# Performance work log

Hardware: AMD Instinct MI355X
Metric: run time of the kernel (lower is better)

Reference implementation:

```python
import jax, jax.numpy as jnp
import numpy as np

DIM = 768
HEADS = 12
HEAD_DIM = DIM // HEADS
HIDDEN = 4 * DIM
EPS = 1e-5


def _ln(x, w, b):
    mu = jnp.mean(x, axis=-1, keepdims=True)
    var = jnp.var(x, axis=-1, keepdims=True)
    return (x - mu) * jax.lax.rsqrt(var + EPS) * w + b


def setup_inputs() -> dict:
    key = jax.random.key(0)
    ks = jax.random.split(key, 8)
    B, N, C = 8, 1024, DIM
    s = 0.02
    return {
        "before": jax.random.normal(ks[0], (B, N, C), jnp.float32),
        "after": jax.random.normal(ks[1], (B, N, C), jnp.float32),
        "norm1_w": jnp.ones((C,), jnp.float32),
        "norm1_b": jnp.zeros((C,), jnp.float32),
        "qkv_w": jax.random.normal(ks[2], (3 * C, C), jnp.float32) * s,
        "hln_w": jnp.ones((HEAD_DIM,), jnp.float32),
        "hln_b": jnp.zeros((HEAD_DIM,), jnp.float32),
        "proj_w": jax.random.normal(ks[3], (C, C), jnp.float32) * s,
        "proj_b": jnp.zeros((C,), jnp.float32),
        "norm2_w": jnp.ones((C,), jnp.float32),
        "norm2_b": jnp.zeros((C,), jnp.float32),
        "fc1_w": jax.random.normal(ks[4], (HIDDEN, C), jnp.float32) * s,
        "fc1_b": jnp.zeros((HIDDEN,), jnp.float32),
        "fc2_w": jax.random.normal(ks[5], (C, HIDDEN), jnp.float32) * s,
        "fc2_b": jnp.zeros((C,), jnp.float32),
    }


def _qkv_normed(x, qkv_w, hln_w, hln_b):
    B, N, C = x.shape
    qkv = x @ qkv_w.T  # (B,N,3C)
    qkv = qkv.reshape(B, N, 3, HEADS, HEAD_DIM).transpose(2, 0, 3, 1, 4)  # (3,B,H,N,hd)
    qkv = _ln(qkv, hln_w, hln_b)  # per-head LayerNorm over head_dim
    return qkv[0], qkv[1], qkv[2]


def _cross_attn(q, k, v, proj_w, proj_b):
    B, H, N, D = q.shape
    scale = D ** (-0.5)
    attn = jax.nn.softmax(jnp.einsum("bhnd,bhmd->bhnm", q, k) * scale, axis=-1)
    ctx = jnp.einsum("bhnm,bhmd->bhnd", attn, v)
    ctx = ctx.transpose(0, 2, 1, 3).reshape(B, N, H * D)
    ctx = ctx @ proj_w.T + proj_b
    # NOTE: original adds q.reshape(B,N,C) WITHOUT transposing heads (faithful)
    return ctx + q.reshape(B, N, H * D)


def _mlp(x, fc1_w, fc1_b, fc2_w, fc2_b):
    h = jax.nn.gelu(x @ fc1_w.T + fc1_b, approximate=False)
    return h @ fc2_w.T + fc2_b


def reference(before, after, norm1_w, norm1_b, qkv_w, hln_w, hln_b, proj_w, proj_b,
              norm2_w, norm2_b, fc1_w, fc1_b, fc2_w, fc2_b):
    before_n = _ln(before, norm1_w, norm1_b)
    after_n = _ln(after, norm1_w, norm1_b)
    q_b, k_b, v_b = _qkv_normed(before_n, qkv_w, hln_w, hln_b)
    q_a, k_a, v_a = _qkv_normed(after_n, qkv_w, hln_w, hln_b)
    context_a = _cross_attn(q_b, k_a, v_a, proj_w, proj_b)  # before attends to after
    context_b = _cross_attn(q_a, k_b, v_b, proj_w, proj_b)  # after attends to before
    before_o = before_n + context_b
    after_o = after_n + context_a
    before_o = before_o + _mlp(_ln(before_o, norm2_w, norm2_b), fc1_w, fc1_b, fc2_w, fc2_b)
    after_o = after_o + _mlp(_ln(after_o, norm2_w, norm2_b), fc1_w, fc1_b, fc2_w, fc2_b)
    return (before_o, after_o)
```

## Files before the change

kernel.cpp:

```cpp
#include <hip/hip_runtime.h>
#include <hip/hip_bf16.h>

typedef unsigned short u16;
typedef __attribute__((ext_vector_type(8))) short bf16x8;
typedef __attribute__((ext_vector_type(4))) float f32x4;

#define DIRSTRIDE 6291456

__device__ __forceinline__ u16 f2bf(float x){
  __hip_bfloat16 h = __float2bfloat16(x);
  return *reinterpret_cast<u16*>(&h);
}
__device__ __forceinline__ float bf2f(u16 u){
  return __uint_as_float(((unsigned int)u) << 16);
}
__device__ __forceinline__ u16 f2bf_fast(float x){
  return (u16)((__float_as_uint(x) + 0x8000u) >> 16);
}

__device__ __forceinline__ void xcd_remap(int& bx, int& by){
  int gx = (int)gridDim.x;
  int lin = (int)blockIdx.x + gx*(int)blockIdx.y;
  int nwg8 = (gx*(int)gridDim.y) >> 3;
  int rl = (lin & 7)*nwg8 + (lin >> 3);
  bx = rl % gx; by = rl / gx;
}

__global__ __launch_bounds__(256) void zero_kernel(float* __restrict__ p, int n){
  int i = blockIdx.x*256 + threadIdx.x;
  if (i < n) p[i] = 0.f;
}

__global__ __launch_bounds__(256) void cvt_kernel(const float* __restrict__ s,
                                                  u16* __restrict__ d, int n){
  int i = blockIdx.x*256 + threadIdx.x;
  if (i < n) d[i] = f2bf(s[i]);
}

__global__ __launch_bounds__(256) void ln_kernel(const float* __restrict__ s0,
    const float* __restrict__ s1, const float* __restrict__ w,
    const float* __restrict__ b, u16* __restrict__ out,
    float* __restrict__ mu_out, float* __restrict__ rs_out){
  int r = blockIdx.x;
  const float* src = (r < 8192) ? (s0 + (size_t)r*768) : (s1 + (size_t)(r-8192)*768);
  int t = threadIdx.x;
  float v0 = src[t], v1 = src[t+256], v2 = src[t+512];
  __shared__ float red[4];
  float s = v0+v1+v2;
  #pragma unroll
  for (int o=32;o;o>>=1) s += __shfl_xor(s,o);
  if ((t&63)==0) red[t>>6] = s;
  __syncthreads();
  float mean = (red[0]+red[1]+red[2]+red[3]) * (1.0f/768.0f);
  float d0=v0-mean, d1=v1-mean, d2=v2-mean;
  float q = d0*d0+d1*d1+d2*d2;
  __syncthreads();
  #pragma unroll
  for (int o=32;o;o>>=1) q += __shfl_xor(q,o);
  if ((t&63)==0) red[t>>6] = q;
  __syncthreads();
  float var = (red[0]+red[1]+red[2]+red[3]) * (1.0f/768.0f);
  float rstd = rsqrtf(var + 1e-5f);
  if (mu_out && t == 0){ mu_out[r] = mean; rs_out[r] = rstd; }
  size_t base = (size_t)r*768;
  out[base+t]     = f2bf(d0*rstd*w[t]     + b[t]);
  out[base+t+256] = f2bf(d1*rstd*w[t+256] + b[t+256]);
  out[base+t+512] = f2bf(d2*rstd*w[t+512] + b[t+512]);
}

__device__ __forceinline__ void stage_tile64(const u16* g, size_t strideK, u16* lds,
                                             int w, int lane){
  #pragma unroll
  for (int i=0;i<4;i++){
    int row = w*32 + i*8 + (lane>>3);
    int cs  = (lane&7) ^ (row&7);
    const u16* gp = g + (size_t)row*strideK + cs*8;
    __builtin_amdgcn_global_load_lds(
        (const __attribute__((address_space(1))) unsigned int*)gp,
        (__attribute__((address_space(3))) unsigned int*)(lds + (w*4+i)*512),
        16, 0, 0);
  }
}

__device__ __forceinline__ void stage_tile64x64(const u16* g, size_t strideK,
                                                u16* lds, int w, int lane){
  #pragma unroll
  for (int i=0;i<2;i++){
    int row = w*16 + i*8 + (lane>>3);
    int cs  = (lane&7) ^ (row&7);
    const u16* gp = g + (size_t)row*strideK + cs*8;
    __builtin_amdgcn_global_load_lds(
        (const __attribute__((address_space(1))) unsigned int*)gp,
        (__attribute__((address_space(3))) unsigned int*)(lds + (w*2+i)*512),
        16, 0, 0);
  }
}

#define SWZ_FRAG(tile, r, c) (*(const bf16x8*)&(tile)[(r)*64 + (((c) ^ ((r)&7)))*8])

template<int EPI>
__global__ __launch_bounds__(256, 4) void gemm_kernel(
    const u16* __restrict__ A, const u16* __restrict__ W, void* Cout,
    const float* __restrict__ bias, const float* resF,
    int M, int N, int K)
{
  __shared__ __attribute__((aligned(16))) u16 sA[128*64];
  __shared__ __attribute__((aligned(16))) u16 sB[128*64];
  int t = threadIdx.x;
  int w = t>>6, lane = t&63, ln = lane&15, quad = lane>>4;
  int bx, by; xcd_remap(bx, by);
  int m0 = by*128, n0 = bx*128;
  int wr = (w>>1)*64, wc = (w&1)*64;
  f32x4 acc[4][4];
  #pragma unroll
  for (int mi=0;mi<4;mi++)
    #pragma unroll
    for (int ni=0;ni<4;ni++) acc[mi][ni] = (f32x4){0.f,0.f,0.f,0.f};
  int KB = K >> 6;
  for (int kb=0;kb<KB;kb++){
    __syncthreads();
    stage_tile64(A + (size_t)m0*K + kb*64, K, sA, w, lane);
    stage_tile64(W + (size_t)n0*K + kb*64, K, sB, w, lane);
    __syncthreads();
    #pragma unroll
    for (int ks=0;ks<2;ks++){
      bf16x8 aF[4], bF[4];
      #pragma unroll
      for (int mi=0;mi<4;mi++) aF[mi] = SWZ_FRAG(sA, wr+mi*16+ln, ks*4+quad);
      #pragma unroll
      for (int ni=0;ni<4;ni++) bF[ni] = SWZ_FRAG(sB, wc+ni*16+ln, ks*4+quad);
      #pragma unroll
      for (int mi=0;mi<4;mi++)
        #pragma unroll
        for (int ni=0;ni<4;ni++)
          acc[mi][ni] = __builtin_amdgcn_mfma_f32_16x16x32_bf16(aF[mi], bF[ni], acc[mi][ni], 0,0,0);
    }
  }
  #pragma unroll
  for (int mi=0;mi<4;mi++){
    #pragma unroll
    for (int ni=0;ni<4;ni++){
      #pragma unroll
      for (int r=0;r<4;r++){
        int row = m0 + wr + mi*16 + quad*4 + r;
        int col = n0 + wc + ni*16 + ln;
        size_t ridx = (size_t)row*N + col;
        float v = acc[mi][ni][r];
        if (EPI == 2){
          v += bias[col];
          v = 0.5f*v*(1.0f + erff(v*0.70710678118654752f));
          ((u16*)Cout)[ridx] = f2bf(v);
        } else {
          float rf = resF[ridx];
          ((float*)Cout)[ridx] = v + bias[col] + rf;
        }
      }
    }
  }
}

__global__ __launch_bounds__(256, 4) void gemm_fc2_kernel(
    const u16* __restrict__ A, const u16* __restrict__ W, float* __restrict__ Cout,
    const float* __restrict__ bias, const float* resF)
{
  const int N = 768, K = 3072, KB = 48;
  __shared__ __attribute__((aligned(16))) u16 sA[128*64];
  __shared__ __attribute__((aligned(16))) u16 sB[64*64];
  int t = threadIdx.x;
  int w = t>>6, lane = t&63, ln = lane&15, quad = lane>>4;
  int bx, by; xcd_remap(bx, by);
  int m0 = by*128, n0 = bx*64;
  int wr = w*32;
  f32x4 acc[2][4];
  #pragma unroll
  for (int mi=0;mi<2;mi++)
    #pragma unroll
    for (int ni=0;ni<4;ni++) acc[mi][ni] = (f32x4){0.f,0.f,0.f,0.f};
  for (int kb=0;kb<KB;kb++){
    __syncthreads();
    stage_tile64(A + (size_t)m0*K + kb*64, K, sA, w, lane);
    stage_tile64x64(W + (size_t)n0*K + kb*64, K, sB, w, lane);
    __syncthreads();
    #pragma unroll
    for (int ks=0;ks<2;ks++){
      bf16x8 aF[2], bF[4];
      #pragma unroll
      for (int mi=0;mi<2;mi++) aF[mi] = SWZ_FRAG(sA, wr+mi*16+ln, ks*4+quad);
      #pragma unroll
      for (int ni=0;ni<4;ni++) bF[ni] = SWZ_FRAG(sB, ni*16+ln, ks*4+quad);
      #pragma unroll
      for (int mi=0;mi<2;mi++)
        #pragma unroll
        for (int ni=0;ni<4;ni++)
          acc[mi][ni] = __builtin_amdgcn_mfma_f32_16x16x32_bf16(aF[mi], bF[ni], acc[mi][ni], 0,0,0);
    }
  }
  #pragma unroll
  for (int mi=0;mi<2;mi++){
    #pragma unroll
    for (int ni=0;ni<4;ni++){
      #pragma unroll
      for (int r=0;r<4;r++){
        int row = m0 + wr + mi*16 + quad*4 + r;
        int col = n0 + ni*16 + ln;
        size_t ridx = (size_t)row*N + col;
        float rf = resF[ridx];
        Cout[ridx] = acc[mi][ni][r] + bias[col] + rf;
      }
    }
  }
}

__global__ __launch_bounds__(256, 4) void gemm_proj_kernel(
    const u16* __restrict__ A, const u16* __restrict__ W, float* Cout,
    const float* __restrict__ bias, const u16* __restrict__ resQ,
    const float* __restrict__ before, const float* __restrict__ after,
    const float* __restrict__ n1w, const float* __restrict__ n1b,
    const float* __restrict__ mu, const float* __restrict__ rstd)
{
  const int K = 768, N = 768, KB = 12;
  __shared__ __attribute__((aligned(16))) u16 sA[128*64];
  __shared__ __attribute__((aligned(16))) u16 sB[128*64];
  int t = threadIdx.x;
  int w = t>>6, lane = t&63, ln = lane&15, quad = lane>>4;
  int bx, by; xcd_remap(bx, by);
  int m0 = by*128, n0 = bx*128;
  int wr = (w>>1)*64, wc = (w&1)*64;
  f32x4 acc[4][4];
  #pragma unroll
  for (int mi=0;mi<4;mi++)
    #pragma unroll
    for (int ni=0;ni<4;ni++) acc[mi][ni] = (f32x4){0.f,0.f,0.f,0.f};
  for (int kb=0;kb<KB;kb++){
    __syncthreads();
    stage_tile64(A + (size_t)m0*K + kb*64, K, sA, w, lane);
    stage_tile64(W + (size_t)n0*K + kb*64, K, sB, w, lane);
    __syncthreads();
    #pragma unroll
    for (int ks=0;ks<2;ks++){
      bf16x8 aF[4], bF[4];
      #pragma unroll
      for (int mi=0;mi<4;mi++) aF[mi] = SWZ_FRAG(sA, wr+mi*16+ln, ks*4+quad);
      #pragma unroll
      for (int ni=0;ni<4;ni++) bF[ni] = SWZ_FRAG(sB, wc+ni*16+ln, ks*4+quad);
      #pragma unroll
      for (int mi=0;mi<4;mi++)
        #pragma unroll
        for (int ni=0;ni<4;ni++)
          acc[mi][ni] = __builtin_amdgcn_mfma_f32_16x16x32_bf16(aF[mi], bF[ni], acc[mi][ni], 0,0,0);
    }
  }
  #pragma unroll
  for (int mi=0;mi<4;mi++){
    #pragma unroll
    for (int ni=0;ni<4;ni++){
      #pragma unroll
      for (int r=0;r<4;r++){
        int row = m0 + wr + mi*16 + quad*4 + r;
        int col = n0 + wc + ni*16 + ln;
        size_t ridx = (size_t)row*N + col;
        int dirout = row >> 13;
        int rem = row & 8191;
        size_t qidx = (size_t)(1-dirout)*DIRSTRIDE + (size_t)rem*768 + col;
        const float* src = dirout ? after : before;
        float xr = (src[(size_t)rem*768 + col] - mu[row]) * rstd[row] * n1w[col] + n1b[col];
        Cout[ridx] = acc[mi][ni][r] + bias[col] + bf2f(resQ[qidx]) + xr;
      }
    }
  }
}

__global__ __launch_bounds__(256, 4) void gemm_qkv_kernel(
    const u16* __restrict__ A, const u16* __restrict__ W,
    const float* __restrict__ hw, const float* __restrict__ hb,
    u16* __restrict__ q, u16* __restrict__ k, u16* __restrict__ vt)
{
  const int K = 768, KB = 12;
  __shared__ __attribute__((aligned(16))) u16 sA[128*64];
  __shared__ __attribute__((aligned(16))) u16 sB[128*64];
  int t = threadIdx.x;
  int w = t>>6, lane = t&63, ln = lane&15, quad = lane>>4;
  int bx, by; xcd_remap(bx, by);
  int m0 = by*128, n0 = bx*128;
  int wr = (w>>1)*64, wc = (w&1)*64;
  f32x4 acc[4][4];
  #pragma unroll
  for (int mi=0;mi<4;mi++)
    #pragma unroll
    for (int ni=0;ni<4;ni++) acc[mi][ni] = (f32x4){0.f,0.f,0.f,0.f};
  for (int kb=0;kb<KB;kb++){
    __syncthreads();
    stage_tile64(A + (size_t)m0*K + kb*64, K, sA, w, lane);
    stage_tile64(W + (size_t)n0*K + kb*64, K, sB, w, lane);
    __syncthreads();
    #pragma unroll
    for (int ks=0;ks<2;ks++){
      bf16x8 aF[4], bF[4];
      #pragma unroll
      for (int mi=0;mi<4;mi++) aF[mi] = SWZ_FRAG(sA, wr+mi*16+ln, ks*4+quad);
      #pragma unroll
      for (int ni=0;ni<4;ni++) bF[ni] = SWZ_FRAG(sB, wc+ni*16+ln, ks*4+quad);
      #pragma unroll
      for (int mi=0;mi<4;mi++)
        #pragma unroll
        for (int ni=0;ni<4;ni++)
          acc[mi][ni] = __builtin_amdgcn_mfma_f32_16x16x32_bf16(aF[mi], bF[ni], acc[mi][ni], 0,0,0);
    }
  }
  int sec = (n0 + wc) >> 6;
  int which = sec / 12, h = sec - which*12;
  float hwv[4], hbv[4];
  #pragma unroll
  for (int ni=0;ni<4;ni++){ hwv[ni] = hw[ni*16+ln]; hbv[ni] = hb[ni*16+ln]; }
  #pragma unroll
  for (int mi=0;mi<4;mi++){
    #pragma unroll
    for (int r=0;r<4;r++){
      float s = acc[mi][0][r]+acc[mi][1][r]+acc[mi][2][r]+acc[mi][3][r];
      #pragma unroll
      for (int ofs=1; ofs<16; ofs<<=1) s += __shfl_xor(s, ofs);
      float mu = s * (1.0f/64.0f);
      float vv = 0.f;
      #pragma unroll
      for (int ni=0;ni<4;ni++){ float d = acc[mi][ni][r]-mu; vv += d*d; }
      #pragma unroll
      for (int ofs=1; ofs<16; ofs<<=1) vv += __shfl_xor(vv, ofs);
      float rstd = rsqrtf(vv*(1.0f/64.0f) + 1e-5f);
      int token = m0 + wr + mi*16 + quad*4 + r;
      int dir = token >> 13, bb = (token>>10)&7, n = token & 1023;
      size_t base = (size_t)dir*DIRSTRIDE + (size_t)bb*786432 + (size_t)h*65536;
      #pragma unroll
      for (int ni=0;ni<4;ni++){
        u16 y = f2bf((acc[mi][ni][r]-mu)*rstd*hwv[ni] + hbv[ni]);
        int hd = ni*16 + ln;
        if (which == 0)      q[base + (size_t)n*64 + hd] = y;
        else if (which == 1) k[base + (size_t)n*64 + hd] = y;
        else                 vt[base + (size_t)hd*1024 + n] = y;
      }
    }
  }
}

__global__ __launch_bounds__(256) void flash_kernel(const u16* __restrict__ qg,
    const u16* __restrict__ kg, const u16* __restrict__ vtg, u16* __restrict__ ctx)
{
  __shared__ __attribute__((aligned(16))) u16 sK[2][64*64];
  __shared__ __attribute__((aligned(16))) u16 sV[2][64*64];
  __shared__ __attribute__((aligned(16))) u16 sP[4*16*72];
  int lin = (int)blockIdx.x + 16*((int)blockIdx.y + 96*(int)blockIdx.z);
  int x8 = lin & 7, jj = lin >> 3;
  int qt = jj & 15;
  int g  = x8 + 8*(jj >> 4);
  int dout = g & 1, bh = g >> 1;
  int b = bh/12, h = bh - b*12;
  size_t qbase = (size_t)(1-dout)*DIRSTRIDE + (size_t)b*786432 + (size_t)h*65536;
  size_t kbase = (size_t)dout*DIRSTRIDE + (size_t)b*786432 + (size_t)h*65536;
  int t = threadIdx.x;
  int w = t>>6, lane = t&63, ln = lane&15, quad = lane>>4;
  const u16* qp = qg + qbase + (size_t)(qt*64 + w*16 + ln)*64 + quad*8;
  bf16x8 aQ0 = *(const bf16x8*)qp;
  bf16x8 aQ1 = *(const bf16x8*)(qp + 32);
  bf16x8 vOne;
  #pragma unroll
  for (int j=0;j<8;j++) vOne[j] = (short)0x3F80;
  f32x4 o[4];
  #pragma unroll
  for (int ni=0;ni<4;ni++) o[ni] = (f32x4){0.f,0.f,0.f,0.f};
  f32x4 oL = (f32x4){0.f,0.f,0.f,0.f};
  u16* pw = &sP[w*16*72];
  const float cs = 0.18033688011112042f;
  stage_tile64x64(kg  + kbase, 64, sK[0], w, lane);
  stage_tile64x64(vtg + kbase, 1024, sV[0], w, lane);
  __syncthreads();
  int cur = 0;
  for (int kt=0;kt<16;kt++){
    if (kt < 15){
      stage_tile64x64(kg  + kbase + (size_t)(kt+1)*4096, 64, sK[cur^1], w, lane);
      stage_tile64x64(vtg + kbase + (size_t)(kt+1)*64, 1024, sV[cur^1], w, lane);
    }
    const u16* sKc = sK[cur];
    const u16* sVc = sV[cur];
    bf16x8 bK[4][2], bV[4][2];
    #pragma unroll
    for (int ni=0;ni<4;ni++){
      int rr = ni*16 + ln;
      bK[ni][0] = SWZ_FRAG(sKc, rr, quad);
      bK[ni][1] = SWZ_FRAG(sKc, rr, 4+quad);
      bV[ni][0] = SWZ_FRAG(sVc, rr, quad);
      bV[ni][1] = SWZ_FRAG(sVc, rr, 4+quad);
    }
    f32x4 s[4];
    __builtin_amdgcn_s_setprio(1);
    #pragma unroll
    for (int ni=0;ni<4;ni++){
      s[ni] = (f32x4){0.f,0.f,0.f,0.f};
      s[ni] = __builtin_amdgcn_mfma_f32_16x16x32_bf16(aQ0, bK[ni][0], s[ni], 0,0,0);
      s[ni] = __builtin_amdgcn_mfma_f32_16x16x32_bf16(aQ1, bK[ni][1], s[ni], 0,0,0);
    }
    __builtin_amdgcn_s_setprio(0);
    #pragma unroll
    for (int ni=0;ni<4;ni++){
      #pragma unroll
      for (int r=0;r<4;r++){
        float p = exp2f(s[ni][r]*cs);
        pw[(quad*4+r)*72 + ni*16 + ln] = f2bf_fast(p);
      }
    }
    bf16x8 aP0 = *(const bf16x8*)&pw[ln*72 + quad*8];
    bf16x8 aP1 = *(const bf16x8*)&pw[ln*72 + 32 + quad*8];
    __builtin_amdgcn_s_setprio(1);
    #pragma unroll
    for (int ni=0;ni<4;ni++){
      o[ni] = __builtin_amdgcn_mfma_f32_16x16x32_bf16(aP0, bV[ni][0], o[ni], 0,0,0);
      o[ni] = __builtin_amdgcn_mfma_f32_16x16x32_bf16(aP1, bV[ni][1], o[ni], 0,0,0);
    }
    oL = __builtin_amdgcn_mfma_f32_16x16x32_bf16(aP0, vOne, oL, 0,0,0);
    oL = __builtin_amdgcn_mfma_f32_16x16x32_bf16(aP1, vOne, oL, 0,0,0);
    __builtin_amdgcn_s_setprio(0);
    __syncthreads();
    cur ^= 1;
  }
  #pragma unroll
  for (int ni=0;ni<4;ni++){
    #pragma unroll
    for (int r=0;r<4;r++){
      int row = qt*64 + w*16 + quad*4 + r;
      float val = o[ni][r] / oL[r];
      ctx[((size_t)dout*8192 + (size_t)b*1024 + row)*768 + h*64 + ni*16 + ln] = f2bf(val);
    }
  }
}

extern "C" void kernel_launch(void* const* d_in, const int* in_sizes, int n_in,
                              void* d_out, int out_size, void* d_ws, size_t ws_size,
                              hipStream_t stream)
{
  const float* before = (const float*)d_in[0];
  const float* after  = (const float*)d_in[1];
  const float* n1w  = (const float*)d_in[2];
  const float* n1b  = (const float*)d_in[3];
  const float* qkvw = (const float*)d_in[4];
  const float* hlnw = (const float*)d_in[5];
  const float* hlnb = (const float*)d_in[6];
  const float* projw= (const float*)d_in[7];
  const float* projb= (const float*)d_in[8];
  const float* n2w  = (const float*)d_in[9];
  const float* n2b  = (const float*)d_in[10];
  const float* fc1w = (const float*)d_in[11];
  const float* fc1b = (const float*)d_in[12];
  const float* fc2w = (const float*)d_in[13];
  const float* fc2b = (const float*)d_in[14];

  const size_t REQUIRED = 114950144;
  if (ws_size < REQUIRED){
    zero_kernel<<<(out_size + 255)/256, 256, 0, stream>>>((float*)d_out, out_size);
    return;
  }

  char* ws = (char*)d_ws;
  u16* xn    = (u16*)(ws + 0);
  u16* ctxb  = (u16*)(ws + 0);
  u16* gbuf  = (u16*)(ws + 0);
  u16* qb    = (u16*)(ws + 25165824);
  u16* kb    = (u16*)(ws + 50331648);
  u16* h1n   = (u16*)(ws + 50331648);
  u16* vtb   = (u16*)(ws + 75497472);
  u16* wqkv  = (u16*)(ws + 100663296);
  u16* wproj = (u16*)(ws + 104202240);
  u16* wfc1  = (u16*)(ws + 105381888);
  u16* wfc2  = (u16*)(ws + 110100480);
  float* mu1  = (float*)(ws + 114819072);
  float* rs1  = (float*)(ws + 114884608);
  float* h1   = (float*)d_out;
  float* outp = (float*)d_out;

  cvt_kernel<<<6912, 256, 0, stream>>>(qkvw, wqkv, 1769472);
  cvt_kernel<<<2304, 256, 0, stream>>>(projw, wproj, 589824);
  cvt_kernel<<<9216, 256, 0, stream>>>(fc1w, wfc1, 2359296);
  cvt_kernel<<<9216, 256, 0, stream>>>(fc2w, wfc2, 2359296);

  ln_kernel<<<16384, 256, 0, stream>>>(before, after, n1w, n1b, xn, mu1, rs1);
  gemm_qkv_kernel<<<dim3(18,128), 256, 0, stream>>>(xn, wqkv, hlnw, hlnb, qb, kb, vtb);
  flash_kernel<<<dim3(16,96,2), 256, 0, stream>>>(qb, kb, vtb, ctxb);
  gemm_proj_kernel<<<dim3(6,128), 256, 0, stream>>>(ctxb, wproj, h1,
      projb, qb, before, after, n1w, n1b, mu1, rs1);
  ln_kernel<<<16384, 256, 0, stream>>>(h1, h1 + (size_t)8192*768, n2w, n2b, h1n,
      nullptr, nullptr);
  for (int c = 0; c < 2; c++){
    size_t off = (size_t)c * 8192 * 768;
    gemm_kernel<2><<<dim3(24,64), 256, 0, stream>>>(h1n + off, wfc1, gbuf,
        fc1b, nullptr, 8192, 3072, 768);
    gemm_fc2_kernel<<<dim3(12,64), 256, 0, stream>>>(gbuf, wfc2, outp + off,
        fc2b, h1 + off);
  }
}
```

Before: 648.2 us.

## Double query rows per wave in flash attention to reuse K/V tiles

Each wave now handles 32 query rows (two 16-row MFMA tiles) instead of 16, so each block covers 128 queries and the grid halves. Every K/V tile staged into LDS and every fragment read feeds twice as many MFMAs, halving K/V global and LDS traffic per query. The output normalization now multiplies by a reciprocal instead of dividing per element. In exchange, register use (accumulators, scores) and the sP buffer double, which may lower occupancy, and the halved block count (1536) reduces parallelism.

```diff
diff --git a/kernel.cpp b/kernel.cpp
--- a/kernel.cpp
+++ b/kernel.cpp
@@ -346,28 +346,34 @@
 {
   __shared__ __attribute__((aligned(16))) u16 sK[2][64*64];
   __shared__ __attribute__((aligned(16))) u16 sV[2][64*64];
-  __shared__ __attribute__((aligned(16))) u16 sP[4*16*72];
-  int lin = (int)blockIdx.x + 16*((int)blockIdx.y + 96*(int)blockIdx.z);
+  __shared__ __attribute__((aligned(16))) u16 sP[4*32*72];
+  int lin = (int)blockIdx.x + 8*((int)blockIdx.y + 96*(int)blockIdx.z);
   int x8 = lin & 7, jj = lin >> 3;
-  int qt = jj & 15;
-  int g  = x8 + 8*(jj >> 4);
+  int qt = jj & 7;
+  int g  = x8 + 8*(jj >> 3);
   int dout = g & 1, bh = g >> 1;
   int b = bh/12, h = bh - b*12;
   size_t qbase = (size_t)(1-dout)*DIRSTRIDE + (size_t)b*786432 + (size_t)h*65536;
   size_t kbase = (size_t)dout*DIRSTRIDE + (size_t)b*786432 + (size_t)h*65536;
   int t = threadIdx.x;
   int w = t>>6, lane = t&63, ln = lane&15, quad = lane>>4;
-  const u16* qp = qg + qbase + (size_t)(qt*64 + w*16 + ln)*64 + quad*8;
-  bf16x8 aQ0 = *(const bf16x8*)qp;
-  bf16x8 aQ1 = *(const bf16x8*)(qp + 32);
+  const u16* qp = qg + qbase + (size_t)(qt*128 + w*32 + ln)*64 + quad*8;
+  bf16x8 aQ[2][2];
+  aQ[0][0] = *(const bf16x8*)qp;
+  aQ[0][1] = *(const bf16x8*)(qp + 32);
+  aQ[1][0] = *(const bf16x8*)(qp + 16*64);
+  aQ[1][1] = *(const bf16x8*)(qp + 16*64 + 32);
   bf16x8 vOne;
   #pragma unroll
   for (int j=0;j<8;j++) vOne[j] = (short)0x3F80;
-  f32x4 o[4];
-  #pragma unroll
-  for (int ni=0;ni<4;ni++) o[ni] = (f32x4){0.f,0.f,0.f,0.f};
-  f32x4 oL = (f32x4){0.f,0.f,0.f,0.f};
-  u16* pw = &sP[w*16*72];
+  f32x4 o[2][4], oL[2];
+  #pragma unroll
+  for (int mi=0;mi<2;mi++){
+    #pragma unroll
+    for (int ni=0;ni<4;ni++) o[mi][ni] = (f32x4){0.f,0.f,0.f,0.f};
+    oL[mi] = (f32x4){0.f,0.f,0.f,0.f};
+  }
+  u16* pw = &sP[w*32*72];
   const float cs = 0.18033688011112042f;
   stage_tile64x64(kg  + kbase, 64, sK[0], w, lane);
   stage_tile64x64(vtg + kbase, 1024, sV[0], w, lane);
@@ -380,53 +386,72 @@
     }
     const u16* sKc = sK[cur];
     const u16* sVc = sV[cur];
-    bf16x8 bK[4][2], bV[4][2];
+    bf16x8 bK[4][2];
     #pragma unroll
     for (int ni=0;ni<4;ni++){
       int rr = ni*16 + ln;
       bK[ni][0] = SWZ_FRAG(sKc, rr, quad);
       bK[ni][1] = SWZ_FRAG(sKc, rr, 4+quad);
+    }
+    f32x4 s[2][4];
+    __builtin_amdgcn_s_setprio(1);
+    #pragma unroll
+    for (int mi=0;mi<2;mi++){
+      #pragma unroll
+      for (int ni=0;ni<4;ni++){
+        s[mi][ni] = (f32x4){0.f,0.f,0.f,0.f};
+        s[mi][ni] = __builtin_amdgcn_mfma_f32_16x16x32_bf16(aQ[mi][0], bK[ni][0], s[mi][ni], 0,0,0);
+        s[mi][ni] = __builtin_amdgcn_mfma_f32_16x16x32_bf16(aQ[mi][1], bK[ni][1], s[mi][ni], 0,0,0);
+      }
+    }
+    __builtin_amdgcn_s_setprio(0);
+    bf16x8 bV[4][2];
+    #pragma unroll
+    for (int ni=0;ni<4;ni++){
+      int rr = ni*16 + ln;
       bV[ni][0] = SWZ_FRAG(sVc, rr, quad);
       bV[ni][1] = SWZ_FRAG(sVc, rr, 4+quad);
     }
-    f32x4 s[4];
+    #pragma unroll
+    for (int mi=0;mi<2;mi++)
+      #pragma unroll
+      for (int ni=0;ni<4;ni++)
+        #pragma unroll
+        for (int r=0;r<4;r++){
+          float p = exp2f(s[mi][ni][r]*cs);
+          pw[(mi*16 + quad*4 + r)*72 + ni*16 + ln] = f2bf_fast(p);
+        }
+    bf16x8 aP[2][2];
+    #pragma unroll
+    for (int mi=0;mi<2;mi++){
+      aP[mi][0] = *(const bf16x8*)&pw[(mi*16+ln)*72 + quad*8];
+      aP[mi][1] = *(const bf16x8*)&pw[(mi*16+ln)*72 + 32 + quad*8];
+    }
     __builtin_amdgcn_s_setprio(1);
     #pragma unroll
-    for (int ni=0;ni<4;ni++){
-      s[ni] = (f32x4){0.f,0.f,0.f,0.f};
-      s[ni] = __builtin_amdgcn_mfma_f32_16x16x32_bf16(aQ0, bK[ni][0], s[ni], 0,0,0);
-      s[ni] = __builtin_amdgcn_mfma_f32_16x16x32_bf16(aQ1, bK[ni][1], s[ni], 0,0,0);
+    for (int mi=0;mi<2;mi++){
+      #pragma unroll
+      for (int ni=0;ni<4;ni++){
+        o[mi][ni] = __builtin_amdgcn_mfma_f32_16x16x32_bf16(aP[mi][0], bV[ni][0], o[mi][ni], 0,0,0);
+        o[mi][ni] = __builtin_amdgcn_mfma_f32_16x16x32_bf16(aP[mi][1], bV[ni][1], o[mi][ni], 0,0,0);
+      }
+      oL[mi] = __builtin_amdgcn_mfma_f32_16x16x32_bf16(aP[mi][0], vOne, oL[mi], 0,0,0);
+      oL[mi] = __builtin_amdgcn_mfma_f32_16x16x32_bf16(aP[mi][1], vOne, oL[mi], 0,0,0);
     }
     __builtin_amdgcn_s_setprio(0);
-    #pragma unroll
-    for (int ni=0;ni<4;ni++){
-      #pragma unroll
-      for (int r=0;r<4;r++){
-        float p = exp2f(s[ni][r]*cs);
-        pw[(quad*4+r)*72 + ni*16 + ln] = f2bf_fast(p);
-      }
-    }
-    bf16x8 aP0 = *(const bf16x8*)&pw[ln*72 + quad*8];
-    bf16x8 aP1 = *(const bf16x8*)&pw[ln*72 + 32 + quad*8];
-    __builtin_amdgcn_s_setprio(1);
-    #pragma unroll
-    for (int ni=0;ni<4;ni++){
-      o[ni] = __builtin_amdgcn_mfma_f32_16x16x32_bf16(aP0, bV[ni][0], o[ni], 0,0,0);
-      o[ni] = __builtin_amdgcn_mfma_f32_16x16x32_bf16(aP1, bV[ni][1], o[ni], 0,0,0);
-    }
-    oL = __builtin_amdgcn_mfma_f32_16x16x32_bf16(aP0, vOne, oL, 0,0,0);
-    oL = __builtin_amdgcn_mfma_f32_16x16x32_bf16(aP1, vOne, oL, 0,0,0);
-    __builtin_amdgcn_s_setprio(0);
     __syncthreads();
     cur ^= 1;
   }
   #pragma unroll
-  for (int ni=0;ni<4;ni++){
+  for (int mi=0;mi<2;mi++){
     #pragma unroll
     for (int r=0;r<4;r++){
-      int row = qt*64 + w*16 + quad*4 + r;
-      float val = o[ni][r] / oL[r];
-      ctx[((size_t)dout*8192 + (size_t)b*1024 + row)*768 + h*64 + ni*16 + ln] = f2bf(val);
+      float inv = 1.0f / oL[mi][r];
+      int row = qt*128 + w*32 + mi*16 + quad*4 + r;
+      size_t obase = ((size_t)dout*8192 + (size_t)b*1024 + row)*768 + h*64;
+      #pragma unroll
+      for (int ni=0;ni<4;ni++)
+        ctx[obase + ni*16 + ln] = f2bf(o[mi][ni][r] * inv);
     }
   }
 }
@@ -481,7 +506,7 @@
 
   ln_kernel<<<16384, 256, 0, stream>>>(before, after, n1w, n1b, xn, mu1, rs1);
   gemm_qkv_kernel<<<dim3(18,128), 256, 0, stream>>>(xn, wqkv, hlnw, hlnb, qb, kb, vtb);
-  flash_kernel<<<dim3(16,96,2), 256, 0, stream>>>(qb, kb, vtb, ctxb);
+  flash_kernel<<<dim3(8,96,2), 256, 0, stream>>>(qb, kb, vtb, ctxb);
   gemm_proj_kernel<<<dim3(6,128), 256, 0, stream>>>(ctxb, wproj, h1,
       projb, qb, before, after, n1w, n1b, mu1, rs1);
   ln_kernel<<<16384, 256, 0, stream>>>(h1, h1 + (size_t)8192*768, n2w, n2b, h1n,
```

Result: faster. 617.3 us (-4.8%).
